# Performance work log

Hardware: AMD Instinct MI355X
Metric: run time of the kernel (lower is better)

## Reference

```python
import jax, jax.numpy as jnp
import numpy as np


def setup_inputs() -> dict:
    key = jax.random.key(0)
    k1, k2 = jax.random.split(key)
    b, c, h, w = 8, 256, 96, 192
    x = jax.random.normal(k1, (b, c, h, w), dtype=jnp.float32)
    y = jax.random.normal(k2, (b, c, h, w), dtype=jnp.float32)
    return {"x": x, "y": y, "max_displacement": 4}


def _correlation(x, y, md):
    # x, y: [B, C, H, W]. Output: [B, K*K, H, W], K = 2*md+1.
    b, c, h, w = x.shape
    K = 2 * md + 1
    # zero-pad y spatially so out-of-bounds displacements contribute 0
    yp = jnp.pad(y, ((0, 0), (0, 0), (md, md), (md, md)))
    # fixed small loop over K*K displacements (81 for md=4)
    outs = [
        jnp.einsum('bchw,bchw->bhw', x, yp[:, :, di:di + h, dj:dj + w])
        for di in range(K) for dj in range(K)
    ]
    out = jnp.stack(outs, axis=1)  # [B, K*K, H, W]
    return out / c


def reference(x, y, max_displacement):
    return _correlation(x, y, max_displacement)
```

## Files before the change

kernel.cpp:

```cpp
#include <hip/hip_runtime.h>
#include <hip/hip_bf16.h>
#include <stdint.h>


using f32x4 = __attribute__((ext_vector_type(4))) float;
using s16x4 = __attribute__((ext_vector_type(4))) short;
using u16x4 = __attribute__((ext_vector_type(4))) unsigned short;

#define C_DIM 256
#define H_DIM 96
#define W_DIM 192
#define HWSZ  (H_DIM * W_DIM)
#define MD 4
#define KD 9
#define CHUNK 32
#define HR 8
#define NTHR 512
#define WTILES 12
#define HQ 12
#define SUB_B 160
#define YROW_B (16 * SUB_B)
#define XROW_B (8 * SUB_B)
#define XBASE  (16 * YROW_B)
#define LDS_BYTES (XBASE + 8 * XROW_B)

static __device__ __forceinline__ unsigned short bf16b(float f) {
  __bf16 h = (__bf16)f;
  unsigned short s; __builtin_memcpy(&s, &h, 2); return s;
}

static __device__ __forceinline__ s16x4 tr16(uint32_t addr) {
  s16x4 d;
  asm volatile("ds_read_b64_tr_b16 %0, %1" : "=v"(d) : "v"(addr));
  return d;
}

__global__ __launch_bounds__(NTHR, 4)
void corr_mfma(const float* __restrict__ xg, const float* __restrict__ yg,
               float* __restrict__ outg) {
  __shared__ __align__(16) char smem[LDS_BYTES];

  const int bid = blockIdx.x;
  const int b   = bid & 7;
  const int rem = bid >> 3;
  const int wt  = rem / HQ;
  const int hq  = rem - wt * HQ;
  const int w0  = wt * 16;
  const int h0  = hq * HR;

  const int tid  = threadIdx.x;
  const int lane = tid & 63;
  const int wv   = tid >> 6;
  const int hi   = lane >> 4;
  const int lm   = lane & 15;

  const uint32_t sbase = (uint32_t)(uintptr_t)&smem[0];

  uint32_t goffY[6], loffY[6], goffX[2], loffX[2];
  uint32_t vmaskY = 0;
#pragma unroll
  for (int i = 0; i < 6; ++i) {
    const int qid = i * NTHR + tid;
    const int q = qid % 6;
    const int c = (qid / 6) & 31;
    const int r = qid / 192;
    const int hg = h0 + r - MD;
    const int sg = w0 - MD + 4 * q;
    const bool ok = (hg >= 0) && (hg < H_DIM) && (sg >= 0) && (sg < W_DIM);
    if (ok) vmaskY |= (1u << i);
    goffY[i] = ok ? (uint32_t)(((b * C_DIM + c) * H_DIM + hg) * W_DIM + sg) : 0u;
    const int s = 4 * q;
    loffY[i] = r * YROW_B + (s >> 4) * (8 * SUB_B) + (c >> 2) * SUB_B
             + (c & 3) * 32 + (s & 15) * 2;
  }
#pragma unroll
  for (int i = 0; i < 2; ++i) {
    const int qid = i * NTHR + tid;
    const int q = qid & 3;
    const int c = (qid >> 2) & 31;
    const int r = qid >> 7;
    goffX[i] = (uint32_t)(((b * C_DIM + c) * H_DIM + (h0 + r)) * W_DIM + (w0 + 4 * q));
    loffX[i] = XBASE + r * XROW_B + (c >> 2) * SUB_B + (c & 3) * 32 + q * 8;
  }

  f32x4 acc[KD][2];
#pragma unroll
  for (int di = 0; di < KD; ++di) {
    acc[di][0] = f32x4{0.f, 0.f, 0.f, 0.f};
    acc[di][1] = f32x4{0.f, 0.f, 0.f, 0.f};
  }

  const uint32_t abase = sbase + XBASE + wv * XROW_B + hi * SUB_B + lm * 8;
  const uint32_t bbase = sbase + wv * YROW_B + hi * SUB_B + lm * 8;

  for (int c0 = 0; c0 < C_DIM; c0 += CHUNK) {
    u16x4 wbuf[8];
#pragma unroll
    for (int i = 0; i < 6; ++i) {
      float4 v = make_float4(0.f, 0.f, 0.f, 0.f);
      if (vmaskY & (1u << i)) v = *(const float4*)(yg + goffY[i] + (uint32_t)c0 * HWSZ);
      wbuf[i] = u16x4{bf16b(v.x), bf16b(v.y), bf16b(v.z), bf16b(v.w)};
    }
#pragma unroll
    for (int i = 0; i < 2; ++i) {
      float4 v = *(const float4*)(xg + goffX[i] + (uint32_t)c0 * HWSZ);
      wbuf[6 + i] = u16x4{bf16b(v.x), bf16b(v.y), bf16b(v.z), bf16b(v.w)};
    }

    __syncthreads();
#pragma unroll
    for (int i = 0; i < 6; ++i) *(u16x4*)(smem + loffY[i]) = wbuf[i];
#pragma unroll
    for (int i = 0; i < 2; ++i) *(u16x4*)(smem + loffX[i]) = wbuf[6 + i];
    __syncthreads();

    s16x4 afr0 = tr16(abase);
    s16x4 afr1 = tr16(abase + 4 * SUB_B);
    s16x4 bc0 = tr16(bbase);
    s16x4 bc1 = tr16(bbase + 4 * SUB_B);
    s16x4 bc2 = tr16(bbase + 8 * SUB_B);
    s16x4 bc3 = tr16(bbase + 12 * SUB_B);
#pragma unroll
    for (int di = 0; di < KD; ++di) {
      s16x4 bn0, bn1, bn2, bn3;
      if (di < 8) {
        const uint32_t bb = bbase + (uint32_t)(di + 1) * YROW_B;
        bn0 = tr16(bb);
        bn1 = tr16(bb + 4 * SUB_B);
        bn2 = tr16(bb + 8 * SUB_B);
        bn3 = tr16(bb + 12 * SUB_B);
        asm volatile("s_waitcnt lgkmcnt(4)" ::: "memory");
      } else {
        asm volatile("s_waitcnt lgkmcnt(0)" ::: "memory");
      }
      __builtin_amdgcn_sched_barrier(0);
      acc[di][0] = __builtin_amdgcn_mfma_f32_16x16x16bf16_1k(afr0, bc0, acc[di][0], 0, 0, 0);
      acc[di][0] = __builtin_amdgcn_mfma_f32_16x16x16bf16_1k(afr1, bc1, acc[di][0], 0, 0, 0);
      acc[di][1] = __builtin_amdgcn_mfma_f32_16x16x16bf16_1k(afr0, bc2, acc[di][1], 0, 0, 0);
      acc[di][1] = __builtin_amdgcn_mfma_f32_16x16x16bf16_1k(afr1, bc3, acc[di][1], 0, 0, 0);
      if (di < 8) { bc0 = bn0; bc1 = bn1; bc2 = bn2; bc3 = bn3; }
    }
  }

  const int h = h0 + wv;
  const float scale = 1.f / 256.f;
#pragma unroll
  for (int di = 0; di < KD; ++di) {
#pragma unroll
    for (int t = 0; t < 2; ++t) {
#pragma unroll
      for (int rg = 0; rg < 4; ++rg) {
        const int m = hi * 4 + rg;
        const int dj = t * 16 + lm - m;
        if (0 <= dj && dj <= 8) {
          outg[((b * (KD * KD) + di * KD + dj) * H_DIM + h) * W_DIM + w0 + m] =
              acc[di][t][rg] * scale;
        }
      }
    }
  }
}

extern "C" void kernel_launch(void* const* d_in, const int* in_sizes, int n_in,
                              void* d_out, int out_size, void* d_ws, size_t ws_size,
                              hipStream_t stream) {
  const float* x = (const float*)d_in[0];
  const float* y = (const float*)d_in[1];
  float* out = (float*)d_out;
  (void)in_sizes; (void)n_in; (void)d_ws; (void)ws_size; (void)out_size;

  const int grid = 8 * HQ * WTILES;
  corr_mfma<<<dim3(grid), dim3(NTHR), 0, stream>>>(x, y, out);
}
```

Baseline: 140.3 us.

## Double-buffer LDS with register prefetch and halve channel chunk size

Channels are now processed in chunks of 16 instead of 32, and the LDS tiles are double-buffered. Global loads for the next chunk are issued before the MFMA loop on the current chunk, so memory latency overlaps with compute. The cost is twice as many chunk iterations, each with two barriers. The smaller SUB_B stride also drops the padding, which may bring back LDS bank conflicts on the transposed reads.

```diff
diff --git a/kernel.cpp b/kernel.cpp
--- a/kernel.cpp
+++ b/kernel.cpp
@@ -13,16 +13,19 @@
 #define HWSZ  (H_DIM * W_DIM)
 #define MD 4
 #define KD 9
-#define CHUNK 32
+#define CHUNK 16
+#define NCHUNK (C_DIM / CHUNK)
 #define HR 8
 #define NTHR 512
 #define WTILES 12
 #define HQ 12
-#define SUB_B 160
-#define YROW_B (16 * SUB_B)
-#define XROW_B (8 * SUB_B)
-#define XBASE  (16 * YROW_B)
-#define LDS_BYTES (XBASE + 8 * XROW_B)
+#define SUB_B 128
+#define YROW_B (8 * SUB_B)
+#define XROW_B (4 * SUB_B)
+#define YSZ    (16 * YROW_B)
+#define XBASE  YSZ
+#define BUFSZ  (YSZ + 8 * XROW_B)
+#define LDS_BYTES (2 * BUFSZ)
 
 static __device__ __forceinline__ unsigned short bf16b(float f) {
   __bf16 h = (__bf16)f;
@@ -56,31 +59,28 @@
 
   const uint32_t sbase = (uint32_t)(uintptr_t)&smem[0];
 
-  uint32_t goffY[6], loffY[6], goffX[2], loffX[2];
-  uint32_t vmaskY = 0;
+  uint32_t goffY[3], loffY[3], goffX, loffX;
+  uint32_t vmY = 0;
 #pragma unroll
-  for (int i = 0; i < 6; ++i) {
+  for (int i = 0; i < 3; ++i) {
     const int qid = i * NTHR + tid;
     const int q = qid % 6;
-    const int c = (qid / 6) & 31;
-    const int r = qid / 192;
+    const int c = (qid / 6) & 15;
+    const int r = qid / 96;
     const int hg = h0 + r - MD;
     const int sg = w0 - MD + 4 * q;
     const bool ok = (hg >= 0) && (hg < H_DIM) && (sg >= 0) && (sg < W_DIM);
-    if (ok) vmaskY |= (1u << i);
+    if (ok) vmY |= (1u << i);
     goffY[i] = ok ? (uint32_t)(((b * C_DIM + c) * H_DIM + hg) * W_DIM + sg) : 0u;
     const int s = 4 * q;
-    loffY[i] = r * YROW_B + (s >> 4) * (8 * SUB_B) + (c >> 2) * SUB_B
-             + (c & 3) * 32 + (s & 15) * 2;
+    loffY[i] = r * YROW_B + (s >> 4) * 512 + (c >> 2) * SUB_B + (c & 3) * 32 + (s & 15) * 2;
   }
-#pragma unroll
-  for (int i = 0; i < 2; ++i) {
-    const int qid = i * NTHR + tid;
-    const int q = qid & 3;
-    const int c = (qid >> 2) & 31;
-    const int r = qid >> 7;
-    goffX[i] = (uint32_t)(((b * C_DIM + c) * H_DIM + (h0 + r)) * W_DIM + (w0 + 4 * q));
-    loffX[i] = XBASE + r * XROW_B + (c >> 2) * SUB_B + (c & 3) * 32 + q * 8;
+  {
+    const int q = tid & 3;
+    const int c = (tid >> 2) & 15;
+    const int r = tid >> 6;
+    goffX = (uint32_t)(((b * C_DIM + c) * H_DIM + (h0 + r)) * W_DIM + (w0 + 4 * q));
+    loffX = XBASE + r * XROW_B + (c >> 2) * SUB_B + (c & 3) * 32 + 8 * q;
   }
 
   f32x4 acc[KD][2];
@@ -93,52 +93,67 @@
   const uint32_t abase = sbase + XBASE + wv * XROW_B + hi * SUB_B + lm * 8;
   const uint32_t bbase = sbase + wv * YROW_B + hi * SUB_B + lm * 8;
 
-  for (int c0 = 0; c0 < C_DIM; c0 += CHUNK) {
-    u16x4 wbuf[8];
+  float4 v[4];
+  u16x4  wreg[4];
+
 #pragma unroll
-    for (int i = 0; i < 6; ++i) {
-      float4 v = make_float4(0.f, 0.f, 0.f, 0.f);
-      if (vmaskY & (1u << i)) v = *(const float4*)(yg + goffY[i] + (uint32_t)c0 * HWSZ);
-      wbuf[i] = u16x4{bf16b(v.x), bf16b(v.y), bf16b(v.z), bf16b(v.w)};
-    }
+  for (int i = 0; i < 3; ++i) {
+    float4 t4 = make_float4(0.f, 0.f, 0.f, 0.f);
+    if (vmY & (1u << i)) t4 = *(const float4*)(yg + goffY[i]);
+    v[i] = t4;
+  }
+  v[3] = *(const float4*)(xg + goffX);
 #pragma unroll
-    for (int i = 0; i < 2; ++i) {
-      float4 v = *(const float4*)(xg + goffX[i] + (uint32_t)c0 * HWSZ);
-      wbuf[6 + i] = u16x4{bf16b(v.x), bf16b(v.y), bf16b(v.z), bf16b(v.w)};
+  for (int i = 0; i < 4; ++i)
+    wreg[i] = u16x4{bf16b(v[i].x), bf16b(v[i].y), bf16b(v[i].z), bf16b(v[i].w)};
+#pragma unroll
+  for (int i = 0; i < 3; ++i) *(u16x4*)(smem + loffY[i]) = wreg[i];
+  *(u16x4*)(smem + loffX) = wreg[3];
+  __syncthreads();
+
+  for (int t = 0; t < NCHUNK; ++t) {
+    if (t + 1 < NCHUNK) {
+      const uint32_t co = (uint32_t)(t + 1) * CHUNK * HWSZ;
+#pragma unroll
+      for (int i = 0; i < 3; ++i) {
+        float4 t4 = make_float4(0.f, 0.f, 0.f, 0.f);
+        if (vmY & (1u << i)) t4 = *(const float4*)(yg + goffY[i] + co);
+        v[i] = t4;
+      }
+      v[3] = *(const float4*)(xg + goffX + co);
     }
 
-    __syncthreads();
-#pragma unroll
-    for (int i = 0; i < 6; ++i) *(u16x4*)(smem + loffY[i]) = wbuf[i];
-#pragma unroll
-    for (int i = 0; i < 2; ++i) *(u16x4*)(smem + loffX[i]) = wbuf[6 + i];
-    __syncthreads();
-
-    s16x4 afr0 = tr16(abase);
-    s16x4 afr1 = tr16(abase + 4 * SUB_B);
-    s16x4 bc0 = tr16(bbase);
-    s16x4 bc1 = tr16(bbase + 4 * SUB_B);
-    s16x4 bc2 = tr16(bbase + 8 * SUB_B);
-    s16x4 bc3 = tr16(bbase + 12 * SUB_B);
+    const uint32_t bo = (uint32_t)(t & 1) * BUFSZ;
+    s16x4 afr = tr16(abase + bo);
+    s16x4 b0 = tr16(bbase + bo);
+    s16x4 b1 = tr16(bbase + bo + 512);
 #pragma unroll
     for (int di = 0; di < KD; ++di) {
-      s16x4 bn0, bn1, bn2, bn3;
+      s16x4 n0, n1;
       if (di < 8) {
-        const uint32_t bb = bbase + (uint32_t)(di + 1) * YROW_B;
-        bn0 = tr16(bb);
-        bn1 = tr16(bb + 4 * SUB_B);
-        bn2 = tr16(bb + 8 * SUB_B);
-        bn3 = tr16(bb + 12 * SUB_B);
-        asm volatile("s_waitcnt lgkmcnt(4)" ::: "memory");
+        const uint32_t bb = bbase + bo + (uint32_t)(di + 1) * YROW_B;
+        n0 = tr16(bb);
+        n1 = tr16(bb + 512);
+        asm volatile("s_waitcnt lgkmcnt(2)" ::: "memory");
       } else {
         asm volatile("s_waitcnt lgkmcnt(0)" ::: "memory");
       }
       __builtin_amdgcn_sched_barrier(0);
-      acc[di][0] = __builtin_amdgcn_mfma_f32_16x16x16bf16_1k(afr0, bc0, acc[di][0], 0, 0, 0);
-      acc[di][0] = __builtin_amdgcn_mfma_f32_16x16x16bf16_1k(afr1, bc1, acc[di][0], 0, 0, 0);
-      acc[di][1] = __builtin_amdgcn_mfma_f32_16x16x16bf16_1k(afr0, bc2, acc[di][1], 0, 0, 0);
-      acc[di][1] = __builtin_amdgcn_mfma_f32_16x16x16bf16_1k(afr1, bc3, acc[di][1], 0, 0, 0);
-      if (di < 8) { bc0 = bn0; bc1 = bn1; bc2 = bn2; bc3 = bn3; }
+      acc[di][0] = __builtin_amdgcn_mfma_f32_16x16x16bf16_1k(afr, b0, acc[di][0], 0, 0, 0);
+      acc[di][1] = __builtin_amdgcn_mfma_f32_16x16x16bf16_1k(afr, b1, acc[di][1], 0, 0, 0);
+      if (di < 8) { b0 = n0; b1 = n1; }
+    }
+
+    if (t + 1 < NCHUNK) {
+#pragma unroll
+      for (int i = 0; i < 4; ++i)
+        wreg[i] = u16x4{bf16b(v[i].x), bf16b(v[i].y), bf16b(v[i].z), bf16b(v[i].w)};
+      __syncthreads();
+      const uint32_t wo = (uint32_t)((t + 1) & 1) * BUFSZ;
+#pragma unroll
+      for (int i = 0; i < 3; ++i) *(u16x4*)(smem + wo + loffY[i]) = wreg[i];
+      *(u16x4*)(smem + wo + loffX) = wreg[3];
+      __syncthreads();
     }
   }
 
```

Result: slower. 156.5 us (+11.5%).
